# Kernel optimization log

Hardware: AMD Instinct MI355X
Metric: run time of the kernel (lower is better)

The kernel has to match this reference:

```python
import jax, jax.numpy as jnp
import numpy as np

D_MODEL = 1024
N_HEAD = 16


def setup_inputs() -> dict:
    key = jax.random.key(0)
    ks = jax.random.split(key, 7)
    B, L, D = 2, 2048, D_MODEL
    s = 0.02
    return {
        "x": jax.random.normal(ks[0], (B, L, D), dtype=jnp.float32),
        "W_kq": jax.random.normal(ks[1], (D, 2 * D), dtype=jnp.float32) * s,
        "b_kq": jax.random.normal(ks[2], (2 * D,), dtype=jnp.float32) * s,
        "W_v": jax.random.normal(ks[3], (D, D), dtype=jnp.float32) * s,
        "b_v": jax.random.normal(ks[4], (D,), dtype=jnp.float32) * s,
        "W_o": jax.random.normal(ks[5], (D, D), dtype=jnp.float32) * s,
        "b_o": jax.random.normal(ks[6], (D,), dtype=jnp.float32) * s,
    }


def reference(x, W_kq, b_kq, W_v, b_v, W_o, b_o):
    B, L, D = x.shape
    H = N_HEAD
    dh = D // H
    kq = x @ W_kq + b_kq            # (B, L, 2D); split order: k first, then q
    k = kq[..., :D].reshape(B, L, H, dh)
    q = kq[..., D:].reshape(B, L, H, dh)
    v = (x @ W_v + b_v).reshape(B, L, H, dh)
    scale = 1.0 / jnp.sqrt(jnp.float32(dh))
    scores = jnp.einsum('blhd,bmhd->bhlm', q, k) * scale  # (B, H, L, L)
    causal = jnp.tril(jnp.ones((L, L), dtype=bool))
    scores = jnp.where(causal, scores, -jnp.inf)
    attn = jax.nn.softmax(scores, axis=-1)
    out = jnp.einsum('bhlm,bmhd->blhd', attn, v).reshape(B, L, D)
    out = out @ W_o + b_o
    return jnp.squeeze(out)
```

## Files before the change

kernel.cpp:

```cpp
#include <hip/hip_runtime.h>
#include <cstdint>


#define LSEQ 2048
#define DM   1024
#define BL   4096

using frag_ab = __attribute__((ext_vector_type(8))) short;
using half8   = __attribute__((ext_vector_type(8))) _Float16;
using half4   = __attribute__((ext_vector_type(4))) _Float16;
using half2_t = __attribute__((ext_vector_type(2))) _Float16;
using fp16x2  = __attribute__((ext_vector_type(2))) __fp16;
using f32x4   = __attribute__((ext_vector_type(4))) float;

__device__ __forceinline__ unsigned short f2bf(float f) {
  unsigned int u = __float_as_uint(f);
  u += 0x7fffu + ((u >> 16) & 1u);
  return (unsigned short)(u >> 16);
}

__device__ __forceinline__ half2_t pkrtz(float a, float b) {
  const fp16x2 r = __builtin_amdgcn_cvt_pkrtz(a, b);
  return __builtin_bit_cast(half2_t, r);
}

__device__ __forceinline__ void load_lds16(const void* g, void* l) {
  __builtin_amdgcn_global_load_lds(
      (const __attribute__((address_space(1))) unsigned int*)g,
      (__attribute__((address_space(3))) unsigned int*)l, 16, 0, 0);
}


__global__ __launch_bounds__(256) void prep_kernel(
    const float* __restrict__ x, unsigned short* __restrict__ xb,
    const float* __restrict__ W_kq, const float* __restrict__ W_v,
    const float* __restrict__ W_o,
    unsigned short* __restrict__ wcat, _Float16* __restrict__ wot)
{
  const int bid = blockIdx.x;
  const int tid = threadIdx.x;

  if (bid < 4096) {
    const int i = bid * 256 + tid;
    const float4 v = *(const float4*)&x[(size_t)i * 4];
    ushort4 o;
    o.x = f2bf(v.x); o.y = f2bf(v.y); o.z = f2bf(v.z); o.w = f2bf(v.w);
    *(ushort4*)&xb[(size_t)i * 4] = o;
    return;
  }

  __shared__ float tile[32][33];
  const int r  = tid >> 3;
  const int c4 = (tid & 7) * 4;

  const float* W;
  int N, nb, kb, which;
  if (bid < 6144) {
    const int b2 = bid - 4096;
    W = W_kq; N = 2048; nb = (b2 & 63) * 32; kb = (b2 >> 6) * 32; which = 0;
  } else if (bid < 7168) {
    const int b2 = bid - 6144;
    W = W_v;  N = 1024; nb = (b2 & 31) * 32; kb = (b2 >> 5) * 32; which = 1;
  } else {
    const int b2 = bid - 7168;
    W = W_o;  N = 1024; nb = (b2 & 31) * 32; kb = (b2 >> 5) * 32; which = 2;
  }

  const float4 v = *(const float4*)&W[(size_t)(kb + r) * N + nb + c4];
  tile[r][c4 + 0] = v.x; tile[r][c4 + 1] = v.y;
  tile[r][c4 + 2] = v.z; tile[r][c4 + 3] = v.w;
  __syncthreads();

  if (which == 2) {
    half4 o;
    o[0] = (_Float16)tile[c4 + 0][r];
    o[1] = (_Float16)tile[c4 + 1][r];
    o[2] = (_Float16)tile[c4 + 2][r];
    o[3] = (_Float16)tile[c4 + 3][r];
    *(half4*)&wot[(size_t)(nb + r) * 1024 + kb + c4] = o;
  } else {
    ushort4 o;
    o.x = f2bf(tile[c4 + 0][r]);
    o.y = f2bf(tile[c4 + 1][r]);
    o.z = f2bf(tile[c4 + 2][r]);
    o.w = f2bf(tile[c4 + 3][r]);
    unsigned short* dst = (which == 0) ? wcat : wcat + 2097152;
    *(ushort4*)&dst[(size_t)(nb + r) * 1024 + kb + c4] = o;
  }
}


__global__ __launch_bounds__(256) void gemm_kqv(
    const unsigned short* __restrict__ A, const unsigned short* __restrict__ Bt,
    const float* __restrict__ b_kq, const float* __restrict__ b_v,
    unsigned short* __restrict__ kqb, _Float16* __restrict__ vtb)
{
  const int tid  = threadIdx.x;
  const int lane = tid & 63;
  const int w    = tid >> 6;
  const int wm   = (w >> 1) * 64;
  const int wn   = (w & 1) * 64;
  const int n0   = blockIdx.x * 128;
  const int m0   = blockIdx.y * 128;
  const int quad = lane >> 4;
  const int l15  = lane & 15;
  const int K    = 1024;

  __shared__ __align__(16) unsigned short As[128 * 64];
  __shared__ __align__(16) unsigned short Bs[128 * 64];

  const int srow = lane >> 3;
  const int sc   = (lane & 7) ^ srow;

  const unsigned short* gA = A  + (size_t)(m0 + w * 32 + srow) * K + sc * 8;
  const unsigned short* gB = Bt + (size_t)(n0 + w * 32 + srow) * K + sc * 8;

  f32x4 acc[4][4] = {};

  for (int k0 = 0; k0 < K; k0 += 64) {
    __syncthreads();
#pragma unroll
    for (int i = 0; i < 4; ++i) {
      load_lds16(gA + (size_t)i * 8 * K + k0, &As[(w * 32 + i * 8) * 64 + lane * 8]);
      load_lds16(gB + (size_t)i * 8 * K + k0, &Bs[(w * 32 + i * 8) * 64 + lane * 8]);
    }
    __syncthreads();
#pragma unroll
    for (int kf = 0; kf < 2; ++kf) {
      frag_ab af[4], bf[4];
#pragma unroll
      for (int t = 0; t < 4; ++t) {
        const int ra = wm + t * 16 + l15;
        const int pa = (kf * 4 + quad) ^ (ra & 7);
        af[t] = *(const frag_ab*)&As[ra * 64 + pa * 8];
        const int rb = wn + t * 16 + l15;
        const int pb = (kf * 4 + quad) ^ (rb & 7);
        bf[t] = *(const frag_ab*)&Bs[rb * 64 + pb * 8];
      }
#pragma unroll
      for (int i = 0; i < 4; ++i)
#pragma unroll
        for (int j = 0; j < 4; ++j)
          acc[i][j] = __builtin_amdgcn_mfma_f32_16x16x32_bf16(
              af[i], bf[j], acc[i][j], 0, 0, 0);
    }
  }

  if (n0 >= 2048) {
#pragma unroll
    for (int i = 0; i < 4; ++i)
#pragma unroll
      for (int j = 0; j < 4; ++j) {
        const int row0 = m0 + wm + i * 16 + quad * 4;
        const int col  = n0 - 2048 + wn + j * 16 + l15;
        const float bv = b_v[col];
        half4 pk;
        pk[0] = (_Float16)(acc[i][j][0] + bv);
        pk[1] = (_Float16)(acc[i][j][1] + bv);
        pk[2] = (_Float16)(acc[i][j][2] + bv);
        pk[3] = (_Float16)(acc[i][j][3] + bv);
        *(half4*)&vtb[(size_t)col * BL + row0] = pk;
      }
  } else {
    const float sc2 = (n0 + wn >= 1024) ? 0.18033688011112042f : 1.0f;
#pragma unroll
    for (int i = 0; i < 4; ++i)
#pragma unroll
      for (int j = 0; j < 4; ++j) {
        const int row0 = m0 + wm + i * 16 + quad * 4;
        const int col  = n0 + wn + j * 16 + l15;
        const float bv = b_kq[col];
#pragma unroll
        for (int r = 0; r < 4; ++r)
          kqb[(size_t)(row0 + r) * 2048 + col] = f2bf((acc[i][j][r] + bv) * sc2);
      }
  }
}


__global__ __launch_bounds__(256, 4) void gemm_out(
    const _Float16* __restrict__ A, const _Float16* __restrict__ Bt,
    const float* __restrict__ bias, float* __restrict__ C)
{
  const int tid  = threadIdx.x;
  const int lane = tid & 63;
  const int w    = tid >> 6;
  const int wm   = (w >> 1) * 64;
  const int wn   = (w & 1) * 32;
  const int n0   = blockIdx.x * 64;
  const int m0   = blockIdx.y * 128;
  const int quad = lane >> 4;
  const int l15  = lane & 15;
  const int K    = 1024;

  __shared__ __align__(16) _Float16 As[128 * 64];
  __shared__ __align__(16) _Float16 Bs[64 * 64];

  const int srow = lane >> 3;
  const int sc   = (lane & 7) ^ srow;

  const _Float16* gA = A  + (size_t)(m0 + w * 32 + srow) * K + sc * 8;
  const _Float16* gB = Bt + (size_t)(n0 + w * 16 + srow) * K + sc * 8;

  f32x4 acc[4][2] = {};

  for (int k0 = 0; k0 < K; k0 += 64) {
    __syncthreads();
#pragma unroll
    for (int i = 0; i < 4; ++i)
      load_lds16(gA + (size_t)i * 8 * K + k0, &As[(w * 32 + i * 8) * 64 + lane * 8]);
#pragma unroll
    for (int i = 0; i < 2; ++i)
      load_lds16(gB + (size_t)i * 8 * K + k0, &Bs[(w * 16 + i * 8) * 64 + lane * 8]);
    __syncthreads();
#pragma unroll
    for (int kf = 0; kf < 2; ++kf) {
      half8 af[4], bf[2];
#pragma unroll
      for (int t = 0; t < 4; ++t) {
        const int ra = wm + t * 16 + l15;
        const int pa = (kf * 4 + quad) ^ (ra & 7);
        af[t] = *(const half8*)&As[ra * 64 + pa * 8];
      }
#pragma unroll
      for (int t = 0; t < 2; ++t) {
        const int rb = wn + t * 16 + l15;
        const int pb = (kf * 4 + quad) ^ (rb & 7);
        bf[t] = *(const half8*)&Bs[rb * 64 + pb * 8];
      }
#pragma unroll
      for (int i = 0; i < 4; ++i)
#pragma unroll
        for (int j = 0; j < 2; ++j)
          acc[i][j] = __builtin_amdgcn_mfma_f32_16x16x32_f16(
              af[i], bf[j], acc[i][j], 0, 0, 0);
    }
  }

#pragma unroll
  for (int i = 0; i < 4; ++i)
#pragma unroll
    for (int j = 0; j < 2; ++j) {
      const int row0 = m0 + wm + i * 16 + quad * 4;
      const int col  = n0 + wn + j * 16 + l15;
      const float bv = bias[col];
#pragma unroll
      for (int r = 0; r < 4; ++r)
        C[(size_t)(row0 + r) * DM + col] = acc[i][j][r] + bv;
    }
}


__global__ __launch_bounds__(256) void attn_mfma(
    const unsigned short* __restrict__ kq, const _Float16* __restrict__ vt,
    _Float16* __restrict__ att)
{
  const int tid  = threadIdx.x;
  const int lane = tid & 63;
  const int w    = tid >> 6;
  const int bx   = blockIdx.x;
  const int qt   = 31 - (bx >> 5);
  const int bh   = bx & 31;
  const int b    = bh >> 4;
  const int h    = bh & 15;
  const int q0   = qt * 64;
  const int quad = lane >> 4;
  const int l15  = lane & 15;

  __shared__ __align__(16) unsigned short Ks[128 * 64];
  __shared__ __align__(16) _Float16      Vs[64 * 128];

#pragma unroll
  for (int i = 0; i < 2; ++i) {
    const int L = i * 256 + tid;
    const int row = L >> 3, c = L & 7;
    const unsigned short* g = kq + (size_t)(b * LSEQ + q0 + row) * 2048
                                 + DM + h * 64 + ((c ^ (row & 7)) * 8);
    load_lds16(g, &Ks[(size_t)L * 8]);
  }
  asm volatile("s_waitcnt vmcnt(0)\n\ts_barrier" ::: "memory");
  frag_ab qa[2];
#pragma unroll
  for (int kf = 0; kf < 2; ++kf) {
    const int row = w * 16 + l15;
    const int c = (kf * 4 + quad) ^ (row & 7);
    qa[kf] = *(const frag_ab*)&Ks[row * 64 + c * 8];
  }
  asm volatile("s_waitcnt lgkmcnt(0)\n\ts_barrier" ::: "memory");

  const int nk = (qt + 2) >> 1;

#define STAGE_K(K0)                                                            \
  {                                                                            \
    _Pragma("unroll")                                                          \
    for (int i = 0; i < 4; ++i) {                                              \
      const int L = i * 256 + tid;                                             \
      const int row = L >> 3, c = L & 7;                                       \
      const unsigned short* g = kq + (size_t)(b * LSEQ + (K0) + row) * 2048    \
                                   + h * 64 + ((c ^ (row & 7)) * 8);           \
      load_lds16(g, &Ks[(size_t)L * 8]);                                       \
    }                                                                          \
  }
#define STAGE_V(K0)                                                            \
  {                                                                            \
    _Pragma("unroll")                                                          \
    for (int i = 0; i < 4; ++i) {                                              \
      const int L = i * 256 + tid;                                             \
      const int row = L >> 4, c16 = L & 15;                                    \
      const _Float16* g = vt + (size_t)(h * 64 + row) * BL                     \
                             + b * LSEQ + (K0) + ((c16 ^ (row & 15)) * 8);     \
      load_lds16(g, &Vs[(size_t)L * 8]);                                       \
    }                                                                          \
  }

  STAGE_K(0);
  STAGE_V(0);

  f32x4 oacc[4] = {};
  float mrow = -3e38f, lrow = 0.f;

  for (int kt = 0; kt < nk; ++kt) {
    const int k0 = kt * 128;
    const bool more = (kt + 1 < nk);

    asm volatile("s_waitcnt vmcnt(4)\n\ts_barrier" ::: "memory");

    f32x4 st[8];
#pragma unroll
    for (int mt = 0; mt < 8; ++mt) {
      f32x4 s = {};
#pragma unroll
      for (int kf = 0; kf < 2; ++kf) {
        const int row = mt * 16 + l15;
        const int c = (kf * 4 + quad) ^ (row & 7);
        const frag_ab kfrag = *(const frag_ab*)&Ks[row * 64 + c * 8];
        s = __builtin_amdgcn_mfma_f32_16x16x32_bf16(kfrag, qa[kf], s, 0, 0, 0);
      }
      st[mt] = s;
    }

    asm volatile("s_waitcnt lgkmcnt(0)\n\ts_barrier" ::: "memory");
    if (more) STAGE_K(k0 + 128);

    if (kt == nk - 1) {
      const int qg = q0 + w * 16 + l15;
#pragma unroll
      for (int mt = 0; mt < 8; ++mt)
#pragma unroll
        for (int r = 0; r < 4; ++r)
          if (k0 + mt * 16 + quad * 4 + r > qg) st[mt][r] = -3e38f;
    }

    float mx = fmaxf(st[0][0], st[0][1]);
    mx = fmaxf(fmaxf(mx, st[0][2]), st[0][3]);
#pragma unroll
    for (int mt = 1; mt < 8; ++mt) {
      mx = fmaxf(fmaxf(mx, st[mt][0]), st[mt][1]);
      mx = fmaxf(fmaxf(mx, st[mt][2]), st[mt][3]);
    }
    mx = fmaxf(mx, __shfl_xor(mx, 16));
    mx = fmaxf(mx, __shfl_xor(mx, 32));

    if (!__all(mx - mrow <= 8.0f)) {
      const float mnew  = fmaxf(mrow, mx);
      const float alpha = __builtin_amdgcn_exp2f(mrow - mnew);
      float aq[4];
#pragma unroll
      for (int r = 0; r < 4; ++r) aq[r] = __shfl(alpha, quad * 4 + r);
#pragma unroll
      for (int dt = 0; dt < 4; ++dt)
#pragma unroll
        for (int r = 0; r < 4; ++r) oacc[dt][r] *= aq[r];
      lrow *= alpha;
      mrow = mnew;
    }

    half4 pf[8];
    float rs0 = 0.f, rs1 = 0.f, rs2 = 0.f, rs3 = 0.f;
#pragma unroll
    for (int mt = 0; mt < 8; ++mt) {
      const float e0 = __builtin_amdgcn_exp2f(st[mt][0] - mrow);
      const float e1 = __builtin_amdgcn_exp2f(st[mt][1] - mrow);
      const float e2 = __builtin_amdgcn_exp2f(st[mt][2] - mrow);
      const float e3 = __builtin_amdgcn_exp2f(st[mt][3] - mrow);
      rs0 += e0; rs1 += e1; rs2 += e2; rs3 += e3;
      const half2_t p01 = pkrtz(e0, e1);
      const half2_t p23 = pkrtz(e2, e3);
      half4 p;
      p[0] = p01[0]; p[1] = p01[1]; p[2] = p23[0]; p[3] = p23[1];
      pf[mt] = p;
    }
    float rsum = (rs0 + rs1) + (rs2 + rs3);
    rsum += __shfl_xor(rsum, 16);
    rsum += __shfl_xor(rsum, 32);
    lrow += rsum;

    if (more) {
      asm volatile("s_waitcnt vmcnt(4)\n\ts_barrier" ::: "memory");
    } else {
      asm volatile("s_waitcnt vmcnt(0)\n\ts_barrier" ::: "memory");
    }

#pragma unroll
    for (int c8 = 0; c8 < 8; ++c8) {
#pragma unroll
      for (int dt = 0; dt < 4; ++dt) {
        const int g16 = 2 * c8 + (quad >> 1);
        const half4 vf = *(const half4*)&Vs[(dt * 16 + l15) * 128
                                            + ((g16 ^ l15) << 3) + ((quad & 1) << 2)];
        oacc[dt] = __builtin_amdgcn_mfma_f32_16x16x16f16(pf[c8], vf, oacc[dt], 0, 0, 0);
      }
    }

    if (more) {
      asm volatile("s_waitcnt lgkmcnt(0)\n\ts_barrier" ::: "memory");
      STAGE_V(k0 + 128);
    }
  }

  float lq[4];
#pragma unroll
  for (int r = 0; r < 4; ++r) lq[r] = 1.0f / __shfl(lrow, quad * 4 + r);
#pragma unroll
  for (int dt = 0; dt < 4; ++dt)
#pragma unroll
    for (int r = 0; r < 4; ++r) {
      const int row = b * LSEQ + q0 + w * 16 + quad * 4 + r;
      const int col = h * 64 + dt * 16 + l15;
      att[(size_t)row * DM + col] = (_Float16)(oacc[dt][r] * lq[r]);
    }
#undef STAGE_K
#undef STAGE_V
}


extern "C" void kernel_launch(void* const* d_in, const int* in_sizes, int n_in,
                              void* d_out, int out_size, void* d_ws, size_t ws_size,
                              hipStream_t stream)
{
  const float* x    = (const float*)d_in[0];
  const float* W_kq = (const float*)d_in[1];
  const float* b_kq = (const float*)d_in[2];
  const float* W_v  = (const float*)d_in[3];
  const float* b_v  = (const float*)d_in[4];
  const float* W_o  = (const float*)d_in[5];
  const float* b_o  = (const float*)d_in[6];

  unsigned short* ws   = (unsigned short*)d_ws;
  unsigned short* xb   = ws;
  unsigned short* wcat = xb   + 4194304;
  _Float16*       wot  = (_Float16*)(wcat + 3145728);
  unsigned short* kqb  = (unsigned short*)(wot + 1048576);
  _Float16*       vtb  = (_Float16*)(kqb + 8388608);
  _Float16*       attb = vtb + 4194304;

  prep_kernel<<<8192, 256, 0, stream>>>(x, xb, W_kq, W_v, W_o, wcat, wot);
  gemm_kqv<<<dim3(24, 32), 256, 0, stream>>>(xb, wcat, b_kq, b_v, kqb, vtb);
  attn_mfma<<<1024, 256, 0, stream>>>(kqb, vtb, attb);
  gemm_out<<<dim3(16, 32), 256, 0, stream>>>(attb, wot, b_o, (float*)d_out);
}
```

Baseline: 183.7 us.

## Overlap next-tile global loads with MFMA in both GEMMs and raise MFMA priority

Both projection GEMMs now read all LDS fragments for a k-tile into registers, barrier, then issue the async global-to-LDS loads for the next tile before running the MFMAs. This hides global load latency behind compute instead of stalling on two syncthreads per iteration. s_setprio raises wave priority around MFMA blocks in the GEMMs and the attention kernel, and the occupancy hints in launch_bounds change (3 for gemm_kqv, 2 for gemm_out). Holding fragments for both k-halves raises register pressure, and the lower occupancy hint could reduce latency hiding.

```diff
diff --git a/kernel.cpp b/kernel.cpp
--- a/kernel.cpp
+++ b/kernel.cpp
@@ -90,7 +90,7 @@
 }
 
 
-__global__ __launch_bounds__(256) void gemm_kqv(
+__global__ __launch_bounds__(256, 3) void gemm_kqv(
     const unsigned short* __restrict__ A, const unsigned short* __restrict__ Bt,
     const float* __restrict__ b_kq, const float* __restrict__ b_v,
     unsigned short* __restrict__ kqb, _Float16* __restrict__ vtb)
@@ -115,36 +115,52 @@
   const unsigned short* gA = A  + (size_t)(m0 + w * 32 + srow) * K + sc * 8;
   const unsigned short* gB = Bt + (size_t)(n0 + w * 32 + srow) * K + sc * 8;
 
+#define STAGE_AB(K0)                                                           \
+  {                                                                            \
+    _Pragma("unroll")                                                          \
+    for (int i = 0; i < 4; ++i) {                                              \
+      load_lds16(gA + (size_t)i * 8 * K + (K0),                                \
+                 &As[(w * 32 + i * 8) * 64 + lane * 8]);                       \
+      load_lds16(gB + (size_t)i * 8 * K + (K0),                                \
+                 &Bs[(w * 32 + i * 8) * 64 + lane * 8]);                       \
+    }                                                                          \
+  }
+
   f32x4 acc[4][4] = {};
 
+  STAGE_AB(0);
+  asm volatile("s_waitcnt vmcnt(0)\n\ts_barrier" ::: "memory");
+
   for (int k0 = 0; k0 < K; k0 += 64) {
-    __syncthreads();
-#pragma unroll
-    for (int i = 0; i < 4; ++i) {
-      load_lds16(gA + (size_t)i * 8 * K + k0, &As[(w * 32 + i * 8) * 64 + lane * 8]);
-      load_lds16(gB + (size_t)i * 8 * K + k0, &Bs[(w * 32 + i * 8) * 64 + lane * 8]);
-    }
-    __syncthreads();
-#pragma unroll
-    for (int kf = 0; kf < 2; ++kf) {
-      frag_ab af[4], bf[4];
+    frag_ab af[2][4], bf[2][4];
+#pragma unroll
+    for (int kf = 0; kf < 2; ++kf)
 #pragma unroll
       for (int t = 0; t < 4; ++t) {
         const int ra = wm + t * 16 + l15;
         const int pa = (kf * 4 + quad) ^ (ra & 7);
-        af[t] = *(const frag_ab*)&As[ra * 64 + pa * 8];
+        af[kf][t] = *(const frag_ab*)&As[ra * 64 + pa * 8];
         const int rb = wn + t * 16 + l15;
         const int pb = (kf * 4 + quad) ^ (rb & 7);
-        bf[t] = *(const frag_ab*)&Bs[rb * 64 + pb * 8];
-      }
+        bf[kf][t] = *(const frag_ab*)&Bs[rb * 64 + pb * 8];
+      }
+    asm volatile("s_waitcnt lgkmcnt(0)\n\ts_barrier" ::: "memory");
+    if (k0 + 64 < K) STAGE_AB(k0 + 64);
+
+    __builtin_amdgcn_s_setprio(1);
+#pragma unroll
+    for (int kf = 0; kf < 2; ++kf)
 #pragma unroll
       for (int i = 0; i < 4; ++i)
 #pragma unroll
         for (int j = 0; j < 4; ++j)
           acc[i][j] = __builtin_amdgcn_mfma_f32_16x16x32_bf16(
-              af[i], bf[j], acc[i][j], 0, 0, 0);
-    }
-  }
+              af[kf][i], bf[kf][j], acc[i][j], 0, 0, 0);
+    __builtin_amdgcn_s_setprio(0);
+
+    asm volatile("s_waitcnt vmcnt(0)\n\ts_barrier" ::: "memory");
+  }
+#undef STAGE_AB
 
   if (n0 >= 2048) {
 #pragma unroll
@@ -178,7 +194,7 @@
 }
 
 
-__global__ __launch_bounds__(256, 4) void gemm_out(
+__global__ __launch_bounds__(256, 2) void gemm_out(
     const _Float16* __restrict__ A, const _Float16* __restrict__ Bt,
     const float* __restrict__ bias, float* __restrict__ C)
 {
@@ -202,40 +218,57 @@
   const _Float16* gA = A  + (size_t)(m0 + w * 32 + srow) * K + sc * 8;
   const _Float16* gB = Bt + (size_t)(n0 + w * 16 + srow) * K + sc * 8;
 
+#define STAGE_AB(K0)                                                           \
+  {                                                                            \
+    _Pragma("unroll")                                                          \
+    for (int i = 0; i < 4; ++i)                                                \
+      load_lds16(gA + (size_t)i * 8 * K + (K0),                                \
+                 &As[(w * 32 + i * 8) * 64 + lane * 8]);                       \
+    _Pragma("unroll")                                                          \
+    for (int i = 0; i < 2; ++i)                                                \
+      load_lds16(gB + (size_t)i * 8 * K + (K0),                                \
+                 &Bs[(w * 16 + i * 8) * 64 + lane * 8]);                       \
+  }
+
   f32x4 acc[4][2] = {};
 
+  STAGE_AB(0);
+  asm volatile("s_waitcnt vmcnt(0)\n\ts_barrier" ::: "memory");
+
   for (int k0 = 0; k0 < K; k0 += 64) {
-    __syncthreads();
-#pragma unroll
-    for (int i = 0; i < 4; ++i)
-      load_lds16(gA + (size_t)i * 8 * K + k0, &As[(w * 32 + i * 8) * 64 + lane * 8]);
-#pragma unroll
-    for (int i = 0; i < 2; ++i)
-      load_lds16(gB + (size_t)i * 8 * K + k0, &Bs[(w * 16 + i * 8) * 64 + lane * 8]);
-    __syncthreads();
+    half8 af[2][4], bf[2][2];
 #pragma unroll
     for (int kf = 0; kf < 2; ++kf) {
-      half8 af[4], bf[2];
 #pragma unroll
       for (int t = 0; t < 4; ++t) {
         const int ra = wm + t * 16 + l15;
         const int pa = (kf * 4 + quad) ^ (ra & 7);
-        af[t] = *(const half8*)&As[ra * 64 + pa * 8];
+        af[kf][t] = *(const half8*)&As[ra * 64 + pa * 8];
       }
 #pragma unroll
       for (int t = 0; t < 2; ++t) {
         const int rb = wn + t * 16 + l15;
         const int pb = (kf * 4 + quad) ^ (rb & 7);
-        bf[t] = *(const half8*)&Bs[rb * 64 + pb * 8];
-      }
+        bf[kf][t] = *(const half8*)&Bs[rb * 64 + pb * 8];
+      }
+    }
+    asm volatile("s_waitcnt lgkmcnt(0)\n\ts_barrier" ::: "memory");
+    if (k0 + 64 < K) STAGE_AB(k0 + 64);
+
+    __builtin_amdgcn_s_setprio(1);
+#pragma unroll
+    for (int kf = 0; kf < 2; ++kf)
 #pragma unroll
       for (int i = 0; i < 4; ++i)
 #pragma unroll
         for (int j = 0; j < 2; ++j)
           acc[i][j] = __builtin_amdgcn_mfma_f32_16x16x32_f16(
-              af[i], bf[j], acc[i][j], 0, 0, 0);
-    }
-  }
+              af[kf][i], bf[kf][j], acc[i][j], 0, 0, 0);
+    __builtin_amdgcn_s_setprio(0);
+
+    asm volatile("s_waitcnt vmcnt(0)\n\ts_barrier" ::: "memory");
+  }
+#undef STAGE_AB
 
 #pragma unroll
   for (int i = 0; i < 4; ++i)
@@ -326,6 +359,7 @@
     asm volatile("s_waitcnt vmcnt(4)\n\ts_barrier" ::: "memory");
 
     f32x4 st[8];
+    __builtin_amdgcn_s_setprio(1);
 #pragma unroll
     for (int mt = 0; mt < 8; ++mt) {
       f32x4 s = {};
@@ -338,6 +372,7 @@
       }
       st[mt] = s;
     }
+    __builtin_amdgcn_s_setprio(0);
 
     asm volatile("s_waitcnt lgkmcnt(0)\n\ts_barrier" ::: "memory");
     if (more) STAGE_K(k0 + 128);
@@ -401,6 +436,7 @@
       asm volatile("s_waitcnt vmcnt(0)\n\ts_barrier" ::: "memory");
     }
 
+    __builtin_amdgcn_s_setprio(1);
 #pragma unroll
     for (int c8 = 0; c8 < 8; ++c8) {
 #pragma unroll
@@ -411,6 +447,7 @@
         oacc[dt] = __builtin_amdgcn_mfma_f32_16x16x16f16(pf[c8], vf, oacc[dt], 0, 0, 0);
       }
     }
+    __builtin_amdgcn_s_setprio(0);
 
     if (more) {
       asm volatile("s_waitcnt lgkmcnt(0)\n\ts_barrier" ::: "memory");
```

Result: faster. 169.4 us (-7.8%).
